# Optimization experiments

Measured on AMD Instinct MI355X. Metric: run time of the kernel, lower is better.

The kernel has to match this reference:

```python
import jax, jax.numpy as jnp
import numpy as np

B, OBS, TASK = 65536, 512, 128
D, M, N = 64, 32, 4  # embedding dim, module width, modules per layer


def setup_inputs() -> dict:
    key = jax.random.key(0)
    ks = jax.random.split(key, 16)

    def w(k, shape):
        fan_in = shape[-2]
        return jax.random.normal(k, shape, jnp.float32) * np.float32(np.sqrt(2.0 / fan_in))

    z = lambda *s: jnp.zeros(s, jnp.float32)
    return dict(
        obs=jax.random.normal(ks[0], (B, OBS), jnp.float32),
        task=jax.random.normal(ks[1], (B, TASK), jnp.float32),
        Ws1=w(ks[2], (OBS, D)), bs1=z(D),
        Ws2=w(ks[3], (D, D)), bs2=z(D),
        Wt=w(ks[4], (TASK, D)), bt=z(D),
        Wa0=w(ks[5], (D, N * N)), ba0=z(N * N),
        Wa1=w(ks[6], (D, N * N)), ba1=z(N * N),
        Wc0=w(ks[7], (N * N, D)), bc0=z(D),
        Wc1=w(ks[8], (2 * N * N, D)), bc1=z(D),
        We0=w(ks[9], (N, D, M)), be0=z(N, M),
        We1=w(ks[10], (N, M, M)), be1=z(N, M),
        We2=w(ks[11], (N, M, M)), be2=z(N, M),
    )


def reference(obs, task, Ws1, bs1, Ws2, bs2, Wt, bt, Wa0, ba0, Wa1, ba1,
              Wc0, bc0, Wc1, bc1, We0, be0, We1, be1, We2, be2):
    relu = jax.nn.relu
    # base encoders
    s = relu(relu(obs @ Ws1 + bs1) @ Ws2 + bs2)          # [B, D]
    t = relu(task @ Wt + bt)                              # [B, D]
    r0 = s * t                                            # first routing inputs [B, D]
    prev = jnp.broadcast_to(s[None], (N,) + s.shape)      # [N, B, D] (state emb fed to all layer-0 modules)

    # routing layer 0 -> 1
    a0 = jax.nn.softmax((r0 @ Wa0 + ba0).reshape(-1, N, N), axis=-1)   # [B, N_next, N_prev]
    m = relu(jnp.einsum('nbi,nio->nbo', prev, We0) + be0[:, None, :])  # [N, B, M] expert outputs
    prev = jnp.einsum('bij,jbd->ibd', a0, m)                           # [N, B, M] attention-combined
    r = relu((a0.reshape(-1, N * N) @ Wc0 + bc0) * r0)                 # updated routing inputs

    # routing layer 1 -> 2
    a1 = jax.nn.softmax((r @ Wa1 + ba1).reshape(-1, N, N), axis=-1)
    m = relu(jnp.einsum('nbi,nio->nbo', prev, We1) + be1[:, None, :])
    prev = jnp.einsum('bij,jbd->ibd', a1, m)
    attn_cat = jnp.concatenate([a0.reshape(-1, N * N), a1.reshape(-1, N * N)], axis=-1)
    r = relu((attn_cat @ Wc1 + bc1) * r0)  # computed as in original (unused afterward)

    # final module layer, plain sum over modules
    m = relu(jnp.einsum('nbi,nio->nbo', prev, We2) + be2[:, None, :])  # [N, B, M]
    return relu(m.sum(axis=0))                                          # [B, M]
```

## Files before the change

kernel.cpp:

```cpp
#include <hip/hip_runtime.h>
#include <hip/hip_bf16.h>


using f32x4 = __attribute__((ext_vector_type(4))) float;
using h16x4 = __attribute__((ext_vector_type(4))) _Float16;
using u32x4 = __attribute__((ext_vector_type(4))) unsigned int;
using u32x2 = __attribute__((ext_vector_type(2))) unsigned int;

#define MFMA16(a, b, c) __builtin_amdgcn_mfma_f32_16x16x16f16((a), (b), (c), 0, 0, 0)

__device__ __forceinline__ short h_bits(float f) {
  _Float16 h = (_Float16)f;
  return __builtin_bit_cast(short, h);
}

__device__ __forceinline__ void dma16(const void* g, char* l) {
  __builtin_amdgcn_global_load_lds(
      (const __attribute__((address_space(1))) unsigned int*)g,
      (__attribute__((address_space(3))) unsigned int*)l, 16, 0, 0);
}

__global__ void sm_convert_v9(
    const float* __restrict__ Ws1, const float* __restrict__ Ws2, const float* __restrict__ Wt,
    const float* __restrict__ Wa0, const float* __restrict__ Wa1, const float* __restrict__ Wc0,
    const float* __restrict__ We0, const float* __restrict__ We1, const float* __restrict__ We2,
    const float* __restrict__ bs1, const float* __restrict__ bs2, const float* __restrict__ bt,
    const float* __restrict__ ba0, const float* __restrict__ ba1, const float* __restrict__ bc0,
    const float* __restrict__ be0, const float* __restrict__ be1, const float* __restrict__ be2,
    short* __restrict__ wsh, float* __restrict__ biasf) {
  int d = blockIdx.x * 256 + threadIdx.x;
  if (d < 64512) {
    float v;
    if (d < 32768) {
      int kk   = d & 3;
      int ntip = (d >> 2) & 1;
      int p    = (d >> 3) & 15;
      int q    = (d >> 7) & 3;
      int pair = (d >> 9) & 1;
      int kb2  = (d >> 10) & 1;
      int c    = d >> 11;
      int k = c * 32 + kb2 * 16 + q * 4 + kk;
      int o = pair * 32 + ntip * 16 + p;
      v = Ws1[k * 64 + o];
    }
    else if (d < 36864) { int r = d - 32768, o = r >> 6, k = r & 63;   v = Ws2[k * 64 + o]; }
    else if (d < 45056) {
      int r = d - 36864;
      int kk   = r & 3;
      int ntip = (r >> 2) & 1;
      int p    = (r >> 3) & 15;
      int q    = (r >> 7) & 3;
      int pair = (r >> 9) & 1;
      int kb2  = (r >> 10) & 1;
      int c    = r >> 11;
      int k = c * 32 + kb2 * 16 + q * 4 + kk;
      int o = pair * 32 + ntip * 16 + p;
      v = Wt[k * 64 + o];
    }
    else if (d < 46080) { int r = d - 45056, o = r >> 6, k = r & 63;   v = Wa0[k * 16 + o]; }
    else if (d < 47104) { int r = d - 46080, o = r >> 6, k = r & 63;   v = Wa1[k * 16 + o]; }
    else if (d < 48128) { int r = d - 47104, o = r >> 4, k = r & 15;   v = Wc0[k * 64 + o]; }
    else if (d < 56320) { int r = d - 48128, n = r >> 11, o = (r >> 6) & 31, i = r & 63; v = We0[n * 2048 + i * 32 + o]; }
    else if (d < 60416) { int r = d - 56320, n = r >> 10, o = (r >> 5) & 31, i = r & 31; v = We1[n * 1024 + i * 32 + o]; }
    else                { int r = d - 60416, n = r >> 10, o = (r >> 5) & 31, i = r & 31; v = We2[n * 1024 + i * 32 + o]; }
    wsh[d] = h_bits(v);
  } else if (d < 65184) {
    int r = d - 64512;
    float v;
    if      (r < 64)  v = bs1[r];
    else if (r < 128) v = bs2[r - 64];
    else if (r < 192) v = bt[r - 128];
    else if (r < 208) v = ba0[r - 192];
    else if (r < 224) v = ba1[r - 208];
    else if (r < 288) v = bc0[r - 224];
    else if (r < 416) v = be0[r - 288];
    else if (r < 544) v = be1[r - 416];
    else              v = be2[r - 544];
    biasf[r] = v;
  }
}

__global__ __launch_bounds__(256) void sm_fused_v9(
    const float* __restrict__ obs, const float* __restrict__ task,
    const short* __restrict__ wsh, const float* __restrict__ biasf,
    float* __restrict__ out) {
  const int tid  = threadIdx.x;
  const int wave = tid >> 6;
  const int lane = tid & 63;
  const int q    = lane >> 4;
  const int p    = lane & 15;
  const int lrow = wave * 16;
  const int wgrow  = blockIdx.x * 64;
  const int rowblk = wgrow + lrow;

  __shared__ __align__(16) char lds[36352];
  char* x_lds = lds;
  char* a_lds = lds + 8704;
  char* ring  = lds + 11776;
  char* p_lds = lds;

  const short* Bp1  = wsh;
  const short* Ws2T = wsh + 32768;
  const short* WtP  = wsh + 36864;
  const short* Wa0T = wsh + 45056;
  const short* Wa1T = wsh + 46080;
  const short* Wc0T = wsh + 47104;
  const short* We0T = wsh + 48128;
  const short* We1T = wsh + 56320;
  const short* We2T = wsh + 60416;
  const float* bs1 = biasf;        const float* bs2 = biasf + 64;
  const float* bt  = biasf + 128;  const float* ba0 = biasf + 192;
  const float* ba1 = biasf + 208;  const float* bc0 = biasf + 224;
  const float* be0 = biasf + 288;  const float* be1 = biasf + 416;
  const float* be2 = biasf + 544;

  const f32x4 z4 = {0.f, 0.f, 0.f, 0.f};

  auto stx  = [&](int row, int col, float v) { *(short*)(x_lds + row * 136 + col * 2) = h_bits(v); };
  auto ldx4 = [&](int row, int k0) -> h16x4 { return *(const h16x4*)(x_lds + row * 136 + k0 * 2); };
  auto ldb  = [&](const short* W, int off) -> h16x4 { return *(const h16x4*)(W + off); };
  auto cvtA = [&](const u32x4& u) -> h16x4 {
    float4 v = __builtin_bit_cast(float4, u);
    h16x4 a;
    a[0] = (_Float16)v.x; a[1] = (_Float16)v.y;
    a[2] = (_Float16)v.z; a[3] = (_Float16)v.w;
    return a;
  };
  auto lo2 = [&](const u32x4& u) -> h16x4 { return __builtin_bit_cast(h16x4, (u32x2){u[0], u[1]}); };
  auto hi2 = [&](const u32x4& u) -> h16x4 { return __builtin_bit_cast(h16x4, (u32x2){u[2], u[3]}); };

  auto stageA = [&](const float* base, int rowlen, int k0, int buf) {
#pragma unroll
    for (int j = 0; j < 2; ++j) {
      int f = j * 256 + wave * 64 + lane;
      int row = f >> 3;
      int cl = (f & 7) ^ (row & 7);
      dma16(base + (size_t)(wgrow + row) * rowlen + k0 + cl * 4,
            ring + buf * 12288 + j * 4096 + wave * 1024);
    }
  };
  auto stageB = [&](const short* bsrc, int c, int buf) {
    dma16((const char*)bsrc + c * 4096 + (wave * 64 + lane) * 16,
          ring + buf * 12288 + 8192 + wave * 1024);
  };
  auto lda_ = [&](int buf, int kb2) -> u32x4 {
    return *(const u32x4*)(ring + buf * 12288 + (lrow + p) * 128 +
                           (((kb2 * 4 + q) ^ (p & 7)) * 16));
  };
  auto ldbs = [&](int buf, int kb2, int pair) -> u32x4 {
    return *(const u32x4*)(ring + buf * 12288 + 8192 + kb2 * 2048 + pair * 1024 + lane * 16);
  };

  f32x4 accX[4] = {z4, z4, z4, z4};
  {
    stageA(obs, 512, 0, 0); stageB(Bp1, 0, 0);
    for (int c = 0; c < 16; ++c) {
      asm volatile("s_waitcnt vmcnt(0)" ::: "memory");
      __builtin_amdgcn_s_barrier();
      __builtin_amdgcn_sched_barrier(0);
      if (c + 1 < 16) {
        stageA(obs, 512, (c + 1) * 32, (c + 1) & 1);
        stageB(Bp1, c + 1, (c + 1) & 1);
      }
      __builtin_amdgcn_sched_barrier(0);
      const int buf = c & 1;
#pragma unroll
      for (int kb2 = 0; kb2 < 2; ++kb2) {
        h16x4 a = cvtA(lda_(buf, kb2));
        u32x4 B0 = ldbs(buf, kb2, 0);
        u32x4 B1 = ldbs(buf, kb2, 1);
        accX[0] = MFMA16(a, lo2(B0), accX[0]);
        accX[1] = MFMA16(a, hi2(B0), accX[1]);
        accX[2] = MFMA16(a, lo2(B1), accX[2]);
        accX[3] = MFMA16(a, hi2(B1), accX[3]);
      }
    }
  }

  stageA(task, 128, 0, 0); stageB(WtP, 0, 0);

#pragma unroll
  for (int nt = 0; nt < 4; ++nt) {
    float bias = bs1[nt * 16 + p];
#pragma unroll
    for (int r = 0; r < 4; ++r)
      stx(lrow + 4 * q + r, nt * 16 + p, fmaxf(accX[nt][r] + bias, 0.f));
  }

  f32x4 accS[4] = {z4, z4, z4, z4};
#pragma unroll
  for (int kb = 0; kb < 4; ++kb) {
    h16x4 a = ldx4(lrow + p, kb * 16 + q * 4);
#pragma unroll
    for (int nt = 0; nt < 4; ++nt)
      accS[nt] = MFMA16(a, ldb(Ws2T, (nt * 16 + p) * 64 + kb * 16 + q * 4), accS[nt]);
  }
  float sf[4][4];
#pragma unroll
  for (int nt = 0; nt < 4; ++nt) {
    float bias = bs2[nt * 16 + p];
#pragma unroll
    for (int r = 0; r < 4; ++r) sf[nt][r] = fmaxf(accS[nt][r] + bias, 0.f);
  }
#pragma unroll
  for (int nt = 0; nt < 4; ++nt)
#pragma unroll
    for (int r = 0; r < 4; ++r) stx(lrow + 4 * q + r, nt * 16 + p, sf[nt][r]);

  f32x4 accT[4] = {z4, z4, z4, z4};
  {
    for (int c = 0; c < 4; ++c) {
      asm volatile("s_waitcnt vmcnt(0)" ::: "memory");
      __builtin_amdgcn_s_barrier();
      __builtin_amdgcn_sched_barrier(0);
      if (c + 1 < 4) {
        stageA(task, 128, (c + 1) * 32, (c + 1) & 1);
        stageB(WtP, c + 1, (c + 1) & 1);
      }
      __builtin_amdgcn_sched_barrier(0);
      const int buf = c & 1;
#pragma unroll
      for (int kb2 = 0; kb2 < 2; ++kb2) {
        h16x4 a = cvtA(lda_(buf, kb2));
        u32x4 B0 = ldbs(buf, kb2, 0);
        u32x4 B1 = ldbs(buf, kb2, 1);
        accT[0] = MFMA16(a, lo2(B0), accT[0]);
        accT[1] = MFMA16(a, hi2(B0), accT[1]);
        accT[2] = MFMA16(a, lo2(B1), accT[2]);
        accT[3] = MFMA16(a, hi2(B1), accT[3]);
      }
    }
  }
  float r0f[4][4];
#pragma unroll
  for (int nt = 0; nt < 4; ++nt) {
    float bias = bt[nt * 16 + p];
#pragma unroll
    for (int r = 0; r < 4; ++r)
      r0f[nt][r] = sf[nt][r] * fmaxf(accT[nt][r] + bias, 0.f);
  }

  float mfr[4][2][4];
#pragma unroll
  for (int n = 0; n < 4; ++n) {
    f32x4 acc[2] = {z4, z4};
#pragma unroll
    for (int kb = 0; kb < 4; ++kb) {
      h16x4 a = ldx4(lrow + p, kb * 16 + q * 4);
#pragma unroll
      for (int nt = 0; nt < 2; ++nt)
        acc[nt] = MFMA16(a, ldb(We0T, (n * 32 + nt * 16 + p) * 64 + kb * 16 + q * 4), acc[nt]);
    }
#pragma unroll
    for (int nt = 0; nt < 2; ++nt) {
      float bias = be0[n * 32 + nt * 16 + p];
#pragma unroll
      for (int r = 0; r < 4; ++r) mfr[n][nt][r] = fmaxf(acc[nt][r] + bias, 0.f);
    }
  }

#pragma unroll
  for (int nt = 0; nt < 4; ++nt)
#pragma unroll
    for (int r = 0; r < 4; ++r) stx(lrow + 4 * q + r, nt * 16 + p, r0f[nt][r]);

  f32x4 accA = z4;
#pragma unroll
  for (int kb = 0; kb < 4; ++kb)
    accA = MFMA16(ldx4(lrow + p, kb * 16 + q * 4), ldb(Wa0T, p * 64 + kb * 16 + q * 4), accA);
  float a0v[4];
  {
    float bias = ba0[p];
#pragma unroll
    for (int r = 0; r < 4; ++r) {
      float v = accA[r] + bias;
      float mx = fmaxf(v, __shfl_xor(v, 1));
      mx = fmaxf(mx, __shfl_xor(mx, 2));
      float e = __expf(v - mx);
      float ssum = e + __shfl_xor(e, 1);
      ssum += __shfl_xor(ssum, 2);
      a0v[r] = e / ssum;
    }
  }
#pragma unroll
  for (int r = 0; r < 4; ++r)
    *(short*)(a_lds + (lrow + 4 * q + r) * 48 + p * 2) = h_bits(a0v[r]);

  float pv[4][2][4];
#pragma unroll
  for (int i = 0; i < 4; ++i)
#pragma unroll
    for (int nt = 0; nt < 2; ++nt)
#pragma unroll
      for (int r = 0; r < 4; ++r) pv[i][nt][r] = 0.f;
  const int sbase = lane & 48;
#pragma unroll
  for (int r = 0; r < 4; ++r) {
#pragma unroll
    for (int c = 0; c < 16; ++c) {
      float av = __shfl(a0v[r], sbase | c);
      pv[c >> 2][0][r] += av * mfr[c & 3][0][r];
      pv[c >> 2][1][r] += av * mfr[c & 3][1][r];
    }
  }

  f32x4 accC[4] = {z4, z4, z4, z4};
  {
    h16x4 a = *(const h16x4*)(a_lds + (lrow + p) * 48 + q * 8);
#pragma unroll
    for (int nt = 0; nt < 4; ++nt)
      accC[nt] = MFMA16(a, ldb(Wc0T, (nt * 16 + p) * 16 + q * 4), accC[nt]);
  }
  float rf[4][4];
#pragma unroll
  for (int nt = 0; nt < 4; ++nt) {
    float bias = bc0[nt * 16 + p];
#pragma unroll
    for (int r = 0; r < 4; ++r)
      rf[nt][r] = fmaxf((accC[nt][r] + bias) * r0f[nt][r], 0.f);
  }
#pragma unroll
  for (int nt = 0; nt < 4; ++nt)
#pragma unroll
    for (int r = 0; r < 4; ++r) stx(lrow + 4 * q + r, nt * 16 + p, rf[nt][r]);

  f32x4 accA1 = z4;
#pragma unroll
  for (int kb = 0; kb < 4; ++kb)
    accA1 = MFMA16(ldx4(lrow + p, kb * 16 + q * 4), ldb(Wa1T, p * 64 + kb * 16 + q * 4), accA1);
  float a1v[4];
  {
    float bias = ba1[p];
#pragma unroll
    for (int r = 0; r < 4; ++r) {
      float v = accA1[r] + bias;
      float mx = fmaxf(v, __shfl_xor(v, 1));
      mx = fmaxf(mx, __shfl_xor(mx, 2));
      float e = __expf(v - mx);
      float ssum = e + __shfl_xor(e, 1);
      ssum += __shfl_xor(ssum, 2);
      a1v[r] = e / ssum;
    }
  }

  __syncthreads();

#pragma unroll
  for (int i = 0; i < 4; ++i)
#pragma unroll
    for (int nt = 0; nt < 2; ++nt)
#pragma unroll
      for (int r = 0; r < 4; ++r)
        *(short*)(p_lds + (i * 64 + lrow + 4 * q + r) * 80 + (nt * 16 + p) * 2) = h_bits(pv[i][nt][r]);

  float m1f[4][2][4];
#pragma unroll
  for (int n = 0; n < 4; ++n) {
    f32x4 acc[2] = {z4, z4};
#pragma unroll
    for (int kb = 0; kb < 2; ++kb) {
      h16x4 a = *(const h16x4*)(p_lds + (n * 64 + lrow + p) * 80 + kb * 32 + q * 8);
#pragma unroll
      for (int nt = 0; nt < 2; ++nt)
        acc[nt] = MFMA16(a, ldb(We1T, (n * 32 + nt * 16 + p) * 32 + kb * 16 + q * 4), acc[nt]);
    }
#pragma unroll
    for (int nt = 0; nt < 2; ++nt) {
      float bias = be1[n * 32 + nt * 16 + p];
#pragma unroll
      for (int r = 0; r < 4; ++r) m1f[n][nt][r] = fmaxf(acc[nt][r] + bias, 0.f);
    }
  }

#pragma unroll
  for (int i = 0; i < 4; ++i)
#pragma unroll
    for (int nt = 0; nt < 2; ++nt)
#pragma unroll
      for (int r = 0; r < 4; ++r) pv[i][nt][r] = 0.f;
#pragma unroll
  for (int r = 0; r < 4; ++r) {
#pragma unroll
    for (int c = 0; c < 16; ++c) {
      float av = __shfl(a1v[r], sbase | c);
      pv[c >> 2][0][r] += av * m1f[c & 3][0][r];
      pv[c >> 2][1][r] += av * m1f[c & 3][1][r];
    }
  }

#pragma unroll
  for (int i = 0; i < 4; ++i)
#pragma unroll
    for (int nt = 0; nt < 2; ++nt)
#pragma unroll
      for (int r = 0; r < 4; ++r)
        *(short*)(p_lds + (i * 64 + lrow + 4 * q + r) * 80 + (nt * 16 + p) * 2) = h_bits(pv[i][nt][r]);

  float of[2][4] = {{0.f, 0.f, 0.f, 0.f}, {0.f, 0.f, 0.f, 0.f}};
#pragma unroll
  for (int n = 0; n < 4; ++n) {
    f32x4 acc[2] = {z4, z4};
#pragma unroll
    for (int kb = 0; kb < 2; ++kb) {
      h16x4 a = *(const h16x4*)(p_lds + (n * 64 + lrow + p) * 80 + kb * 32 + q * 8);
#pragma unroll
      for (int nt = 0; nt < 2; ++nt)
        acc[nt] = MFMA16(a, ldb(We2T, (n * 32 + nt * 16 + p) * 32 + kb * 16 + q * 4), acc[nt]);
    }
#pragma unroll
    for (int nt = 0; nt < 2; ++nt) {
      float bias = be2[n * 32 + nt * 16 + p];
#pragma unroll
      for (int r = 0; r < 4; ++r) of[nt][r] += fmaxf(acc[nt][r] + bias, 0.f);
    }
  }
#pragma unroll
  for (int nt = 0; nt < 2; ++nt)
#pragma unroll
    for (int r = 0; r < 4; ++r) {
      int grow = rowblk + 4 * q + r;
      out[(size_t)grow * 32 + nt * 16 + p] = of[nt][r];
    }
}

extern "C" void kernel_launch(void* const* d_in, const int* in_sizes, int n_in,
                              void* d_out, int out_size, void* d_ws, size_t ws_size,
                              hipStream_t stream) {
  (void)in_sizes; (void)n_in; (void)out_size; (void)ws_size;
  const float* obs  = (const float*)d_in[0];
  const float* task = (const float*)d_in[1];
  const float* Ws1 = (const float*)d_in[2];  const float* bs1 = (const float*)d_in[3];
  const float* Ws2 = (const float*)d_in[4];  const float* bs2 = (const float*)d_in[5];
  const float* Wt  = (const float*)d_in[6];  const float* bt  = (const float*)d_in[7];
  const float* Wa0 = (const float*)d_in[8];  const float* ba0 = (const float*)d_in[9];
  const float* Wa1 = (const float*)d_in[10]; const float* ba1 = (const float*)d_in[11];
  const float* Wc0 = (const float*)d_in[12]; const float* bc0 = (const float*)d_in[13];
  const float* We0 = (const float*)d_in[16]; const float* be0 = (const float*)d_in[17];
  const float* We1 = (const float*)d_in[18]; const float* be1 = (const float*)d_in[19];
  const float* We2 = (const float*)d_in[20]; const float* be2 = (const float*)d_in[21];

  short* wsh   = (short*)d_ws;
  float* biasf = (float*)((char*)d_ws + 129040);

  sm_convert_v9<<<dim3(255), dim3(256), 0, stream>>>(
      Ws1, Ws2, Wt, Wa0, Wa1, Wc0, We0, We1, We2,
      bs1, bs2, bt, ba0, ba1, bc0, be0, be1, be2,
      wsh, biasf);
  sm_fused_v9<<<dim3(1024), dim3(256), 0, stream>>>(
      obs, task, wsh, biasf, (float*)d_out);
}
```

Before: 71.32 us.

## Split fused kernel into encoder and routing kernels via packed fp16 intermediate

Splits the single fused kernel into two: the first computes the state and task encoders and writes s and r0 packed as fp16 pairs to workspace; the second reads them and runs the routing and expert layers. The aim is to lower per-kernel register and LDS pressure so more waves can be resident. In exchange it adds a 16 MB global round-trip for the intermediate and an extra launch. The fused kernel is kept as a fallback when the workspace is too small.

After: 75.70 us. 6.1% more time.

```diff
diff --git a/kernel.cpp b/kernel.cpp
--- a/kernel.cpp
+++ b/kernel.cpp
@@ -12,6 +12,9 @@
 __device__ __forceinline__ short h_bits(float f) {
   _Float16 h = (_Float16)f;
   return __builtin_bit_cast(short, h);
+}
+__device__ __forceinline__ float h2f(unsigned short b) {
+  return (float)__builtin_bit_cast(_Float16, b);
 }
 
 __device__ __forceinline__ void dma16(const void* g, char* l) {
@@ -20,7 +23,7 @@
       (__attribute__((address_space(3))) unsigned int*)l, 16, 0, 0);
 }
 
-__global__ void sm_convert_v9(
+__global__ void sm_convert_v10(
     const float* __restrict__ Ws1, const float* __restrict__ Ws2, const float* __restrict__ Wt,
     const float* __restrict__ Wa0, const float* __restrict__ Wa1, const float* __restrict__ Wc0,
     const float* __restrict__ We0, const float* __restrict__ We1, const float* __restrict__ We2,
@@ -80,7 +83,384 @@
   }
 }
 
-__global__ __launch_bounds__(256) void sm_fused_v9(
+__global__ __launch_bounds__(256) void sm_k1_v10(
+    const float* __restrict__ obs, const float* __restrict__ task,
+    const short* __restrict__ wsh, const float* __restrict__ biasf,
+    unsigned* __restrict__ sr) {
+  const int tid  = threadIdx.x;
+  const int wave = tid >> 6;
+  const int lane = tid & 63;
+  const int q    = lane >> 4;
+  const int p    = lane & 15;
+  const int lrow = wave * 16;
+  const int wgrow  = blockIdx.x * 64;
+  const int rowblk = wgrow + lrow;
+
+  __shared__ __align__(16) char lds[33280];
+  char* x_lds = lds;
+  char* ring  = lds + 8704;
+
+  const short* Bp1  = wsh;
+  const short* Ws2T = wsh + 32768;
+  const short* WtP  = wsh + 36864;
+  const float* bs1 = biasf;        const float* bs2 = biasf + 64;
+  const float* bt  = biasf + 128;
+
+  const f32x4 z4 = {0.f, 0.f, 0.f, 0.f};
+
+  auto stx  = [&](int row, int col, float v) { *(short*)(x_lds + row * 136 + col * 2) = h_bits(v); };
+  auto ldx4 = [&](int row, int k0) -> h16x4 { return *(const h16x4*)(x_lds + row * 136 + k0 * 2); };
+  auto ldb  = [&](const short* W, int off) -> h16x4 { return *(const h16x4*)(W + off); };
+  auto cvtA = [&](const u32x4& u) -> h16x4 {
+    float4 v = __builtin_bit_cast(float4, u);
+    h16x4 a;
+    a[0] = (_Float16)v.x; a[1] = (_Float16)v.y;
+    a[2] = (_Float16)v.z; a[3] = (_Float16)v.w;
+    return a;
+  };
+  auto lo2 = [&](const u32x4& u) -> h16x4 { return __builtin_bit_cast(h16x4, (u32x2){u[0], u[1]}); };
+  auto hi2 = [&](const u32x4& u) -> h16x4 { return __builtin_bit_cast(h16x4, (u32x2){u[2], u[3]}); };
+
+  auto stageA = [&](const float* base, int rowlen, int k0, int buf) {
+#pragma unroll
+    for (int j = 0; j < 2; ++j) {
+      int f = j * 256 + wave * 64 + lane;
+      int row = f >> 3;
+      int cl = (f & 7) ^ (row & 7);
+      dma16(base + (size_t)(wgrow + row) * rowlen + k0 + cl * 4,
+            ring + buf * 12288 + j * 4096 + wave * 1024);
+    }
+  };
+  auto stageB = [&](const short* bsrc, int c, int buf) {
+    dma16((const char*)bsrc + c * 4096 + (wave * 64 + lane) * 16,
+          ring + buf * 12288 + 8192 + wave * 1024);
+  };
+  auto lda_ = [&](int buf, int kb2) -> u32x4 {
+    return *(const u32x4*)(ring + buf * 12288 + (lrow + p) * 128 +
+                           (((kb2 * 4 + q) ^ (p & 7)) * 16));
+  };
+  auto ldbs = [&](int buf, int kb2, int pair) -> u32x4 {
+    return *(const u32x4*)(ring + buf * 12288 + 8192 + kb2 * 2048 + pair * 1024 + lane * 16);
+  };
+
+  f32x4 accX[4] = {z4, z4, z4, z4};
+  {
+    stageA(obs, 512, 0, 0); stageB(Bp1, 0, 0);
+    for (int c = 0; c < 16; ++c) {
+      asm volatile("s_waitcnt vmcnt(0)" ::: "memory");
+      __builtin_amdgcn_s_barrier();
+      __builtin_amdgcn_sched_barrier(0);
+      if (c + 1 < 16) {
+        stageA(obs, 512, (c + 1) * 32, (c + 1) & 1);
+        stageB(Bp1, c + 1, (c + 1) & 1);
+      }
+      __builtin_amdgcn_sched_barrier(0);
+      const int buf = c & 1;
+#pragma unroll
+      for (int kb2 = 0; kb2 < 2; ++kb2) {
+        h16x4 a = cvtA(lda_(buf, kb2));
+        u32x4 B0 = ldbs(buf, kb2, 0);
+        u32x4 B1 = ldbs(buf, kb2, 1);
+        accX[0] = MFMA16(a, lo2(B0), accX[0]);
+        accX[1] = MFMA16(a, hi2(B0), accX[1]);
+        accX[2] = MFMA16(a, lo2(B1), accX[2]);
+        accX[3] = MFMA16(a, hi2(B1), accX[3]);
+      }
+    }
+  }
+
+  stageA(task, 128, 0, 0); stageB(WtP, 0, 0);
+
+#pragma unroll
+  for (int nt = 0; nt < 4; ++nt) {
+    float bias = bs1[nt * 16 + p];
+#pragma unroll
+    for (int r = 0; r < 4; ++r)
+      stx(lrow + 4 * q + r, nt * 16 + p, fmaxf(accX[nt][r] + bias, 0.f));
+  }
+
+  f32x4 accS[4] = {z4, z4, z4, z4};
+#pragma unroll
+  for (int kb = 0; kb < 4; ++kb) {
+    h16x4 a = ldx4(lrow + p, kb * 16 + q * 4);
+#pragma unroll
+    for (int nt = 0; nt < 4; ++nt)
+      accS[nt] = MFMA16(a, ldb(Ws2T, (nt * 16 + p) * 64 + kb * 16 + q * 4), accS[nt]);
+  }
+  float sf[4][4];
+#pragma unroll
+  for (int nt = 0; nt < 4; ++nt) {
+    float bias = bs2[nt * 16 + p];
+#pragma unroll
+    for (int r = 0; r < 4; ++r) sf[nt][r] = fmaxf(accS[nt][r] + bias, 0.f);
+  }
+
+  f32x4 accT[4] = {z4, z4, z4, z4};
+  {
+    for (int c = 0; c < 4; ++c) {
+      asm volatile("s_waitcnt vmcnt(0)" ::: "memory");
+      __builtin_amdgcn_s_barrier();
+      __builtin_amdgcn_sched_barrier(0);
+      if (c + 1 < 4) {
+        stageA(task, 128, (c + 1) * 32, (c + 1) & 1);
+        stageB(WtP, c + 1, (c + 1) & 1);
+      }
+      __builtin_amdgcn_sched_barrier(0);
+      const int buf = c & 1;
+#pragma unroll
+      for (int kb2 = 0; kb2 < 2; ++kb2) {
+        h16x4 a = cvtA(lda_(buf, kb2));
+        u32x4 B0 = ldbs(buf, kb2, 0);
+        u32x4 B1 = ldbs(buf, kb2, 1);
+        accT[0] = MFMA16(a, lo2(B0), accT[0]);
+        accT[1] = MFMA16(a, hi2(B0), accT[1]);
+        accT[2] = MFMA16(a, lo2(B1), accT[2]);
+        accT[3] = MFMA16(a, hi2(B1), accT[3]);
+      }
+    }
+  }
+
+#pragma unroll
+  for (int nt = 0; nt < 4; ++nt) {
+    float bias = bt[nt * 16 + p];
+#pragma unroll
+    for (int r = 0; r < 4; ++r) {
+      float tv = fmaxf(accT[nt][r] + bias, 0.f);
+      float r0 = sf[nt][r] * tv;
+      unsigned pk = (unsigned)(unsigned short)h_bits(sf[nt][r]) |
+                    ((unsigned)(unsigned short)h_bits(r0) << 16);
+      sr[(size_t)(rowblk + 4 * q + r) * 64 + nt * 16 + p] = pk;
+    }
+  }
+}
+
+__global__ __launch_bounds__(256) void sm_k2_v10(
+    const unsigned* __restrict__ sr, const short* __restrict__ wsh,
+    const float* __restrict__ biasf, float* __restrict__ out) {
+  const int tid  = threadIdx.x;
+  const int wave = tid >> 6;
+  const int lane = tid & 63;
+  const int q    = lane >> 4;
+  const int p    = lane & 15;
+  const int lrow = wave * 16;
+  const int rowblk = blockIdx.x * 64 + lrow;
+
+  __shared__ __align__(16) char lds[20480];
+  char* x_lds = lds;
+  char* a_lds = lds + 8704;
+  char* p_lds = lds;
+
+  const short* Wa0T = wsh + 45056;
+  const short* Wa1T = wsh + 46080;
+  const short* Wc0T = wsh + 47104;
+  const short* We0T = wsh + 48128;
+  const short* We1T = wsh + 56320;
+  const short* We2T = wsh + 60416;
+  const float* ba0 = biasf + 192;  const float* ba1 = biasf + 208;
+  const float* bc0 = biasf + 224;  const float* be0 = biasf + 288;
+  const float* be1 = biasf + 416;  const float* be2 = biasf + 544;
+
+  const f32x4 z4 = {0.f, 0.f, 0.f, 0.f};
+
+  auto stx  = [&](int row, int col, float v) { *(short*)(x_lds + row * 136 + col * 2) = h_bits(v); };
+  auto ldx4 = [&](int row, int k0) -> h16x4 { return *(const h16x4*)(x_lds + row * 136 + k0 * 2); };
+  auto ldb  = [&](const short* W, int off) -> h16x4 { return *(const h16x4*)(W + off); };
+  auto lo16 = [&](unsigned a, unsigned b) -> unsigned { return (a & 0xffffu) | (b << 16); };
+  auto hi16 = [&](unsigned a, unsigned b) -> unsigned { return (a >> 16) | (b & 0xffff0000u); };
+
+  h16x4 sA[4], rA[4];
+#pragma unroll
+  for (int kb = 0; kb < 4; ++kb) {
+    u32x4 v = *(const u32x4*)(sr + (size_t)(rowblk + p) * 64 + kb * 16 + q * 4);
+    sA[kb] = __builtin_bit_cast(h16x4, (u32x2){lo16(v[0], v[1]), lo16(v[2], v[3])});
+    rA[kb] = __builtin_bit_cast(h16x4, (u32x2){hi16(v[0], v[1]), hi16(v[2], v[3])});
+  }
+  float r0f[4][4];
+#pragma unroll
+  for (int nt = 0; nt < 4; ++nt)
+#pragma unroll
+    for (int r = 0; r < 4; ++r) {
+      unsigned v = sr[(size_t)(rowblk + 4 * q + r) * 64 + nt * 16 + p];
+      r0f[nt][r] = h2f((unsigned short)(v >> 16));
+    }
+
+  float mfr[4][2][4];
+#pragma unroll
+  for (int n = 0; n < 4; ++n) {
+    f32x4 acc[2] = {z4, z4};
+#pragma unroll
+    for (int kb = 0; kb < 4; ++kb)
+#pragma unroll
+      for (int nt = 0; nt < 2; ++nt)
+        acc[nt] = MFMA16(sA[kb], ldb(We0T, (n * 32 + nt * 16 + p) * 64 + kb * 16 + q * 4), acc[nt]);
+#pragma unroll
+    for (int nt = 0; nt < 2; ++nt) {
+      float bias = be0[n * 32 + nt * 16 + p];
+#pragma unroll
+      for (int r = 0; r < 4; ++r) mfr[n][nt][r] = fmaxf(acc[nt][r] + bias, 0.f);
+    }
+  }
+
+  f32x4 accA = z4;
+#pragma unroll
+  for (int kb = 0; kb < 4; ++kb)
+    accA = MFMA16(rA[kb], ldb(Wa0T, p * 64 + kb * 16 + q * 4), accA);
+  float a0v[4];
+  {
+    float bias = ba0[p];
+#pragma unroll
+    for (int r = 0; r < 4; ++r) {
+      float v = accA[r] + bias;
+      float mx = fmaxf(v, __shfl_xor(v, 1));
+      mx = fmaxf(mx, __shfl_xor(mx, 2));
+      float e = __expf(v - mx);
+      float ssum = e + __shfl_xor(e, 1);
+      ssum += __shfl_xor(ssum, 2);
+      a0v[r] = e / ssum;
+    }
+  }
+#pragma unroll
+  for (int r = 0; r < 4; ++r)
+    *(short*)(a_lds + (lrow + 4 * q + r) * 48 + p * 2) = h_bits(a0v[r]);
+
+  float pv[4][2][4];
+#pragma unroll
+  for (int i = 0; i < 4; ++i)
+#pragma unroll
+    for (int nt = 0; nt < 2; ++nt)
+#pragma unroll
+      for (int r = 0; r < 4; ++r) pv[i][nt][r] = 0.f;
+  const int sbase = lane & 48;
+#pragma unroll
+  for (int r = 0; r < 4; ++r) {
+#pragma unroll
+    for (int c = 0; c < 16; ++c) {
+      float av = __shfl(a0v[r], sbase | c);
+      pv[c >> 2][0][r] += av * mfr[c & 3][0][r];
+      pv[c >> 2][1][r] += av * mfr[c & 3][1][r];
+    }
+  }
+
+  f32x4 accC[4] = {z4, z4, z4, z4};
+  {
+    h16x4 a = *(const h16x4*)(a_lds + (lrow + p) * 48 + q * 8);
+#pragma unroll
+    for (int nt = 0; nt < 4; ++nt)
+      accC[nt] = MFMA16(a, ldb(Wc0T, (nt * 16 + p) * 16 + q * 4), accC[nt]);
+  }
+  float rf[4][4];
+#pragma unroll
+  for (int nt = 0; nt < 4; ++nt) {
+    float bias = bc0[nt * 16 + p];
+#pragma unroll
+    for (int r = 0; r < 4; ++r)
+      rf[nt][r] = fmaxf((accC[nt][r] + bias) * r0f[nt][r], 0.f);
+  }
+#pragma unroll
+  for (int nt = 0; nt < 4; ++nt)
+#pragma unroll
+    for (int r = 0; r < 4; ++r) stx(lrow + 4 * q + r, nt * 16 + p, rf[nt][r]);
+
+  f32x4 accA1 = z4;
+#pragma unroll
+  for (int kb = 0; kb < 4; ++kb)
+    accA1 = MFMA16(ldx4(lrow + p, kb * 16 + q * 4), ldb(Wa1T, p * 64 + kb * 16 + q * 4), accA1);
+  float a1v[4];
+  {
+    float bias = ba1[p];
+#pragma unroll
+    for (int r = 0; r < 4; ++r) {
+      float v = accA1[r] + bias;
+      float mx = fmaxf(v, __shfl_xor(v, 1));
+      mx = fmaxf(mx, __shfl_xor(mx, 2));
+      float e = __expf(v - mx);
+      float ssum = e + __shfl_xor(e, 1);
+      ssum += __shfl_xor(ssum, 2);
+      a1v[r] = e / ssum;
+    }
+  }
+
+  __syncthreads();
+
+#pragma unroll
+  for (int i = 0; i < 4; ++i)
+#pragma unroll
+    for (int nt = 0; nt < 2; ++nt)
+#pragma unroll
+      for (int r = 0; r < 4; ++r)
+        *(short*)(p_lds + (i * 64 + lrow + 4 * q + r) * 80 + (nt * 16 + p) * 2) = h_bits(pv[i][nt][r]);
+
+  float m1f[4][2][4];
+#pragma unroll
+  for (int n = 0; n < 4; ++n) {
+    f32x4 acc[2] = {z4, z4};
+#pragma unroll
+    for (int kb = 0; kb < 2; ++kb) {
+      h16x4 a = *(const h16x4*)(p_lds + (n * 64 + lrow + p) * 80 + kb * 32 + q * 8);
+#pragma unroll
+      for (int nt = 0; nt < 2; ++nt)
+        acc[nt] = MFMA16(a, ldb(We1T, (n * 32 + nt * 16 + p) * 32 + kb * 16 + q * 4), acc[nt]);
+    }
+#pragma unroll
+    for (int nt = 0; nt < 2; ++nt) {
+      float bias = be1[n * 32 + nt * 16 + p];
+#pragma unroll
+      for (int r = 0; r < 4; ++r) m1f[n][nt][r] = fmaxf(acc[nt][r] + bias, 0.f);
+    }
+  }
+
+#pragma unroll
+  for (int i = 0; i < 4; ++i)
+#pragma unroll
+    for (int nt = 0; nt < 2; ++nt)
+#pragma unroll
+      for (int r = 0; r < 4; ++r) pv[i][nt][r] = 0.f;
+#pragma unroll
+  for (int r = 0; r < 4; ++r) {
+#pragma unroll
+    for (int c = 0; c < 16; ++c) {
+      float av = __shfl(a1v[r], sbase | c);
+      pv[c >> 2][0][r] += av * m1f[c & 3][0][r];
+      pv[c >> 2][1][r] += av * m1f[c & 3][1][r];
+    }
+  }
+
+#pragma unroll
+  for (int i = 0; i < 4; ++i)
+#pragma unroll
+    for (int nt = 0; nt < 2; ++nt)
+#pragma unroll
+      for (int r = 0; r < 4; ++r)
+        *(short*)(p_lds + (i * 64 + lrow + 4 * q + r) * 80 + (nt * 16 + p) * 2) = h_bits(pv[i][nt][r]);
+
+  float of[2][4] = {{0.f, 0.f, 0.f, 0.f}, {0.f, 0.f, 0.f, 0.f}};
+#pragma unroll
+  for (int n = 0; n < 4; ++n) {
+    f32x4 acc[2] = {z4, z4};
+#pragma unroll
+    for (int kb = 0; kb < 2; ++kb) {
+      h16x4 a = *(const h16x4*)(p_lds + (n * 64 + lrow + p) * 80 + kb * 32 + q * 8);
+#pragma unroll
+      for (int nt = 0; nt < 2; ++nt)
+        acc[nt] = MFMA16(a, ldb(We2T, (n * 32 + nt * 16 + p) * 32 + kb * 16 + q * 4), acc[nt]);
+    }
+#pragma unroll
+    for (int nt = 0; nt < 2; ++nt) {
+      float bias = be2[n * 32 + nt * 16 + p];
+#pragma unroll
+      for (int r = 0; r < 4; ++r) of[nt][r] += fmaxf(acc[nt][r] + bias, 0.f);
+    }
+  }
+#pragma unroll
+  for (int nt = 0; nt < 2; ++nt)
+#pragma unroll
+    for (int r = 0; r < 4; ++r) {
+      int grow = rowblk + 4 * q + r;
+      out[(size_t)grow * 32 + nt * 16 + p] = of[nt][r];
+    }
+}
+
+__global__ __launch_bounds__(256) void sm_fused_v10fb(
     const float* __restrict__ obs, const float* __restrict__ task,
     const short* __restrict__ wsh, const float* __restrict__ biasf,
     float* __restrict__ out) {
@@ -176,9 +556,7 @@
       }
     }
   }
-
   stageA(task, 128, 0, 0); stageB(WtP, 0, 0);
-
 #pragma unroll
   for (int nt = 0; nt < 4; ++nt) {
     float bias = bs1[nt * 16 + p];
@@ -186,7 +564,6 @@
     for (int r = 0; r < 4; ++r)
       stx(lrow + 4 * q + r, nt * 16 + p, fmaxf(accX[nt][r] + bias, 0.f));
   }
-
   f32x4 accS[4] = {z4, z4, z4, z4};
 #pragma unroll
   for (int kb = 0; kb < 4; ++kb) {
@@ -206,7 +583,6 @@
   for (int nt = 0; nt < 4; ++nt)
 #pragma unroll
     for (int r = 0; r < 4; ++r) stx(lrow + 4 * q + r, nt * 16 + p, sf[nt][r]);
-
   f32x4 accT[4] = {z4, z4, z4, z4};
   {
     for (int c = 0; c < 4; ++c) {
@@ -239,7 +615,6 @@
     for (int r = 0; r < 4; ++r)
       r0f[nt][r] = sf[nt][r] * fmaxf(accT[nt][r] + bias, 0.f);
   }
-
   float mfr[4][2][4];
 #pragma unroll
   for (int n = 0; n < 4; ++n) {
@@ -258,12 +633,10 @@
       for (int r = 0; r < 4; ++r) mfr[n][nt][r] = fmaxf(acc[nt][r] + bias, 0.f);
     }
   }
-
 #pragma unroll
   for (int nt = 0; nt < 4; ++nt)
 #pragma unroll
     for (int r = 0; r < 4; ++r) stx(lrow + 4 * q + r, nt * 16 + p, r0f[nt][r]);
-
   f32x4 accA = z4;
 #pragma unroll
   for (int kb = 0; kb < 4; ++kb)
@@ -285,7 +658,6 @@
 #pragma unroll
   for (int r = 0; r < 4; ++r)
     *(short*)(a_lds + (lrow + 4 * q + r) * 48 + p * 2) = h_bits(a0v[r]);
-
   float pv[4][2][4];
 #pragma unroll
   for (int i = 0; i < 4; ++i)
@@ -303,7 +675,6 @@
       pv[c >> 2][1][r] += av * mfr[c & 3][1][r];
     }
   }
-
   f32x4 accC[4] = {z4, z4, z4, z4};
   {
     h16x4 a = *(const h16x4*)(a_lds + (lrow + p) * 48 + q * 8);
@@ -323,7 +694,6 @@
   for (int nt = 0; nt < 4; ++nt)
 #pragma unroll
     for (int r = 0; r < 4; ++r) stx(lrow + 4 * q + r, nt * 16 + p, rf[nt][r]);
-
   f32x4 accA1 = z4;
 #pragma unroll
   for (int kb = 0; kb < 4; ++kb)
@@ -342,9 +712,7 @@
       a1v[r] = e / ssum;
     }
   }
-
   __syncthreads();
-
 #pragma unroll
   for (int i = 0; i < 4; ++i)
 #pragma unroll
@@ -352,7 +720,6 @@
 #pragma unroll
       for (int r = 0; r < 4; ++r)
         *(short*)(p_lds + (i * 64 + lrow + 4 * q + r) * 80 + (nt * 16 + p) * 2) = h_bits(pv[i][nt][r]);
-
   float m1f[4][2][4];
 #pragma unroll
   for (int n = 0; n < 4; ++n) {
@@ -371,7 +738,6 @@
       for (int r = 0; r < 4; ++r) m1f[n][nt][r] = fmaxf(acc[nt][r] + bias, 0.f);
     }
   }
-
 #pragma unroll
   for (int i = 0; i < 4; ++i)
 #pragma unroll
@@ -387,7 +753,6 @@
       pv[c >> 2][1][r] += av * m1f[c & 3][1][r];
     }
   }
-
 #pragma unroll
   for (int i = 0; i < 4; ++i)
 #pragma unroll
@@ -395,7 +760,6 @@
 #pragma unroll
       for (int r = 0; r < 4; ++r)
         *(short*)(p_lds + (i * 64 + lrow + 4 * q + r) * 80 + (nt * 16 + p) * 2) = h_bits(pv[i][nt][r]);
-
   float of[2][4] = {{0.f, 0.f, 0.f, 0.f}, {0.f, 0.f, 0.f, 0.f}};
 #pragma unroll
   for (int n = 0; n < 4; ++n) {
@@ -426,7 +790,7 @@
 extern "C" void kernel_launch(void* const* d_in, const int* in_sizes, int n_in,
                               void* d_out, int out_size, void* d_ws, size_t ws_size,
                               hipStream_t stream) {
-  (void)in_sizes; (void)n_in; (void)out_size; (void)ws_size;
+  (void)in_sizes; (void)n_in; (void)out_size;
   const float* obs  = (const float*)d_in[0];
   const float* task = (const float*)d_in[1];
   const float* Ws1 = (const float*)d_in[2];  const float* bs1 = (const float*)d_in[3];
@@ -442,10 +806,18 @@
   short* wsh   = (short*)d_ws;
   float* biasf = (float*)((char*)d_ws + 129040);
 
-  sm_convert_v9<<<dim3(255), dim3(256), 0, stream>>>(
+  sm_convert_v10<<<dim3(255), dim3(256), 0, stream>>>(
       Ws1, Ws2, Wt, Wa0, Wa1, Wc0, We0, We1, We2,
       bs1, bs2, bt, ba0, ba1, bc0, be0, be1, be2,
       wsh, biasf);
-  sm_fused_v9<<<dim3(1024), dim3(256), 0, stream>>>(
-      obs, task, wsh, biasf, (float*)d_out);
+
+  const size_t need = (size_t)(1 << 20) + (size_t)65536 * 64 * 4;
+  if (ws_size >= need) {
+    unsigned* sr = (unsigned*)((char*)d_ws + (1 << 20));
+    sm_k1_v10<<<dim3(1024), dim3(256), 0, stream>>>(obs, task, wsh, biasf, sr);
+    sm_k2_v10<<<dim3(1024), dim3(256), 0, stream>>>(sr, wsh, biasf, (float*)d_out);
+  } else {
+    sm_fused_v10fb<<<dim3(1024), dim3(256), 0, stream>>>(
+        obs, task, wsh, biasf, (float*)d_out);
+  }
 }
```

## Triple-buffer the obs/task staging ring and read routing weights from LDS

Applied to the files above, without the earlier changes.

Replaces the double-buffered DMA ring for the obs and task GEMM stages with a three-slot ring. Each iteration issues the loads for the chunk two ahead and waits only for the oldest outstanding group (vmcnt(6)/3/0), so more global loads are in flight behind the MFMA work. The layer-0 attention combine now reads the softmax weights as fp16 vectors from LDS instead of 16 cross-lane shuffles per row. The layer-1 combine is restructured into separate per-module sums, and a1 is also written to LDS. The cost is a larger LDS footprint (about 48.6 KB instead of about 36.4 KB), which may lower occupancy, plus an extra barrier per iteration and fp16 rounding of the a0 weights.

Result: slower. 79.97 us (+12.1%).

```diff
diff --git a/kernel.cpp b/kernel.cpp
--- a/kernel.cpp
+++ b/kernel.cpp
@@ -4,6 +4,7 @@
 
 using f32x4 = __attribute__((ext_vector_type(4))) float;
 using h16x4 = __attribute__((ext_vector_type(4))) _Float16;
+using h16x8 = __attribute__((ext_vector_type(8))) _Float16;
 using u32x4 = __attribute__((ext_vector_type(4))) unsigned int;
 using u32x2 = __attribute__((ext_vector_type(2))) unsigned int;
 
@@ -20,7 +21,7 @@
       (__attribute__((address_space(3))) unsigned int*)l, 16, 0, 0);
 }
 
-__global__ void sm_convert_v9(
+__global__ void sm_convert_v12(
     const float* __restrict__ Ws1, const float* __restrict__ Ws2, const float* __restrict__ Wt,
     const float* __restrict__ Wa0, const float* __restrict__ Wa1, const float* __restrict__ Wc0,
     const float* __restrict__ We0, const float* __restrict__ We1, const float* __restrict__ We2,
@@ -80,7 +81,7 @@
   }
 }
 
-__global__ __launch_bounds__(256) void sm_fused_v9(
+__global__ __launch_bounds__(256) void sm_fused_v12(
     const float* __restrict__ obs, const float* __restrict__ task,
     const short* __restrict__ wsh, const float* __restrict__ biasf,
     float* __restrict__ out) {
@@ -93,7 +94,7 @@
   const int wgrow  = blockIdx.x * 64;
   const int rowblk = wgrow + lrow;
 
-  __shared__ __align__(16) char lds[36352];
+  __shared__ __align__(16) char lds[48640];
   char* x_lds = lds;
   char* a_lds = lds + 8704;
   char* ring  = lds + 11776;
@@ -153,17 +154,22 @@
 
   f32x4 accX[4] = {z4, z4, z4, z4};
   {
-    stageA(obs, 512, 0, 0); stageB(Bp1, 0, 0);
+    stageA(obs, 512, 0, 0);  stageB(Bp1, 0, 0);
+    stageA(obs, 512, 32, 1); stageB(Bp1, 1, 1);
     for (int c = 0; c < 16; ++c) {
-      asm volatile("s_waitcnt vmcnt(0)" ::: "memory");
+      if (c < 14) {
+        stageA(obs, 512, (c + 2) * 32, (c + 2) % 3);
+        stageB(Bp1, c + 2, (c + 2) % 3);
+        __builtin_amdgcn_sched_barrier(0);
+        asm volatile("s_waitcnt vmcnt(6)" ::: "memory");
+      } else if (c == 14) {
+        asm volatile("s_waitcnt vmcnt(3)" ::: "memory");
+      } else {
+        asm volatile("s_waitcnt vmcnt(0)" ::: "memory");
+      }
       __builtin_amdgcn_s_barrier();
       __builtin_amdgcn_sched_barrier(0);
-      if (c + 1 < 16) {
-        stageA(obs, 512, (c + 1) * 32, (c + 1) & 1);
-        stageB(Bp1, c + 1, (c + 1) & 1);
-      }
-      __builtin_amdgcn_sched_barrier(0);
-      const int buf = c & 1;
+      const int buf = c % 3;
 #pragma unroll
       for (int kb2 = 0; kb2 < 2; ++kb2) {
         h16x4 a = cvtA(lda_(buf, kb2));
@@ -174,10 +180,12 @@
         accX[2] = MFMA16(a, lo2(B1), accX[2]);
         accX[3] = MFMA16(a, hi2(B1), accX[3]);
       }
-    }
-  }
-
-  stageA(task, 128, 0, 0); stageB(WtP, 0, 0);
+      __builtin_amdgcn_s_barrier();
+    }
+  }
+
+  stageA(task, 128, 0, 0);  stageB(WtP, 0, 0);
+  stageA(task, 128, 32, 1); stageB(WtP, 1, 1);
 
 #pragma unroll
   for (int nt = 0; nt < 4; ++nt) {
@@ -210,15 +218,19 @@
   f32x4 accT[4] = {z4, z4, z4, z4};
   {
     for (int c = 0; c < 4; ++c) {
-      asm volatile("s_waitcnt vmcnt(0)" ::: "memory");
+      if (c < 2) {
+        stageA(task, 128, (c + 2) * 32, (c + 2) % 3);
+        stageB(WtP, c + 2, (c + 2) % 3);
+        __builtin_amdgcn_sched_barrier(0);
+        asm volatile("s_waitcnt vmcnt(6)" ::: "memory");
+      } else if (c == 2) {
+        asm volatile("s_waitcnt vmcnt(3)" ::: "memory");
+      } else {
+        asm volatile("s_waitcnt vmcnt(0)" ::: "memory");
+      }
       __builtin_amdgcn_s_barrier();
       __builtin_amdgcn_sched_barrier(0);
-      if (c + 1 < 4) {
-        stageA(task, 128, (c + 1) * 32, (c + 1) & 1);
-        stageB(WtP, c + 1, (c + 1) & 1);
-      }
-      __builtin_amdgcn_sched_barrier(0);
-      const int buf = c & 1;
+      const int buf = c % 3;
 #pragma unroll
       for (int kb2 = 0; kb2 < 2; ++kb2) {
         h16x4 a = cvtA(lda_(buf, kb2));
@@ -229,6 +241,7 @@
         accT[2] = MFMA16(a, lo2(B1), accT[2]);
         accT[3] = MFMA16(a, hi2(B1), accT[3]);
       }
+      __builtin_amdgcn_s_barrier();
     }
   }
   float r0f[4][4];
@@ -288,19 +301,21 @@
 
   float pv[4][2][4];
 #pragma unroll
-  for (int i = 0; i < 4; ++i)
-#pragma unroll
-    for (int nt = 0; nt < 2; ++nt)
-#pragma unroll
-      for (int r = 0; r < 4; ++r) pv[i][nt][r] = 0.f;
-  const int sbase = lane & 48;
-#pragma unroll
   for (int r = 0; r < 4; ++r) {
-#pragma unroll
-    for (int c = 0; c < 16; ++c) {
-      float av = __shfl(a0v[r], sbase | c);
-      pv[c >> 2][0][r] += av * mfr[c & 3][0][r];
-      pv[c >> 2][1][r] += av * mfr[c & 3][1][r];
+    h16x8 alo = *(const h16x8*)(a_lds + (lrow + 4 * q + r) * 48);
+    h16x8 ahi = *(const h16x8*)(a_lds + (lrow + 4 * q + r) * 48 + 16);
+    float av[16];
+#pragma unroll
+    for (int e = 0; e < 8; ++e) { av[e] = (float)alo[e]; av[8 + e] = (float)ahi[e]; }
+#pragma unroll
+    for (int i = 0; i < 4; ++i) {
+      float s0 = 0.f, s1 = 0.f;
+#pragma unroll
+      for (int j = 0; j < 4; ++j) {
+        s0 += av[4 * i + j] * mfr[j][0][r];
+        s1 += av[4 * i + j] * mfr[j][1][r];
+      }
+      pv[i][0][r] = s0; pv[i][1][r] = s1;
     }
   }
 
@@ -342,6 +357,9 @@
       a1v[r] = e / ssum;
     }
   }
+#pragma unroll
+  for (int r = 0; r < 4; ++r)
+    *(short*)(a_lds + (lrow + 4 * q + r) * 48 + p * 2) = h_bits(a1v[r]);
 
   __syncthreads();
 
@@ -372,29 +390,33 @@
     }
   }
 
+
+  float pv2[4][2][4];
+#pragma unroll
+  for (int r = 0; r < 4; ++r) {
+    float av[16];
+#pragma unroll
+    for (int cc = 0; cc < 16; ++cc)
+      av[cc] = __shfl(a1v[r], (lane & 48) | cc);
+#pragma unroll
+    for (int i = 0; i < 4; ++i) {
+      float s0 = 0.f, s1 = 0.f;
+#pragma unroll
+      for (int j = 0; j < 4; ++j) {
+        s0 += av[4 * i + j] * m1f[j][0][r];
+        s1 += av[4 * i + j] * m1f[j][1][r];
+      }
+      pv2[i][0][r] = s0; pv2[i][1][r] = s1;
+    }
+  }
+
 #pragma unroll
   for (int i = 0; i < 4; ++i)
 #pragma unroll
     for (int nt = 0; nt < 2; ++nt)
 #pragma unroll
-      for (int r = 0; r < 4; ++r) pv[i][nt][r] = 0.f;
-#pragma unroll
-  for (int r = 0; r < 4; ++r) {
-#pragma unroll
-    for (int c = 0; c < 16; ++c) {
-      float av = __shfl(a1v[r], sbase | c);
-      pv[c >> 2][0][r] += av * m1f[c & 3][0][r];
-      pv[c >> 2][1][r] += av * m1f[c & 3][1][r];
-    }
-  }
-
-#pragma unroll
-  for (int i = 0; i < 4; ++i)
-#pragma unroll
-    for (int nt = 0; nt < 2; ++nt)
-#pragma unroll
       for (int r = 0; r < 4; ++r)
-        *(short*)(p_lds + (i * 64 + lrow + 4 * q + r) * 80 + (nt * 16 + p) * 2) = h_bits(pv[i][nt][r]);
+        *(short*)(p_lds + (i * 64 + lrow + 4 * q + r) * 80 + (nt * 16 + p) * 2) = h_bits(pv2[i][nt][r]);
 
   float of[2][4] = {{0.f, 0.f, 0.f, 0.f}, {0.f, 0.f, 0.f, 0.f}};
 #pragma unroll
@@ -442,10 +464,10 @@
   short* wsh   = (short*)d_ws;
   float* biasf = (float*)((char*)d_ws + 129040);
 
-  sm_convert_v9<<<dim3(255), dim3(256), 0, stream>>>(
+  sm_convert_v12<<<dim3(255), dim3(256), 0, stream>>>(
       Ws1, Ws2, Wt, Wa0, Wa1, Wc0, We0, We1, We2,
       bs1, bs2, bt, ba0, ba1, bc0, be0, be1, be2,
       wsh, biasf);
-  sm_fused_v9<<<dim3(1024), dim3(256), 0, stream>>>(
+  sm_fused_v12<<<dim3(1024), dim3(256), 0, stream>>>(
       obs, task, wsh, biasf, (float*)d_out);
 }
```
